# Kernel optimization log

Hardware: AMD Instinct MI355X
Metric: run time of the kernel (lower is better)

## Reference

```python
import jax, jax.numpy as jnp
import numpy as np

D_MODEL = 1024
D_HEAD = 64
B, S = 4, 2048


def setup_inputs() -> dict:
    key = jax.random.key(0)
    ks = jax.random.split(key, 4)
    scale = 1.0 / np.sqrt(D_MODEL)
    return {
        "embeddings": jax.random.normal(ks[0], (B, S, D_MODEL), dtype=jnp.float32),
        "Wq": jax.random.normal(ks[1], (D_MODEL, D_HEAD), dtype=jnp.float32) * scale,
        "bq": jnp.zeros((D_HEAD,), dtype=jnp.float32),
        "Wk": jax.random.normal(ks[2], (D_MODEL, D_HEAD), dtype=jnp.float32) * scale,
        "bk": jnp.zeros((D_HEAD,), dtype=jnp.float32),
        "Wv": jax.random.normal(ks[3], (D_MODEL, D_HEAD), dtype=jnp.float32) * scale,
        "bv": jnp.zeros((D_HEAD,), dtype=jnp.float32),
    }


def reference(embeddings, Wq, bq, Wk, bk, Wv, bv):
    # Q, K, V projections: (b, s, d_head)
    Q = embeddings @ Wq + bq
    K = embeddings @ Wk + bk
    V = embeddings @ Wv + bv
    # scaled scores: (b, s, s)
    scores = jnp.einsum("bqd,bkd->bqk", Q, K) / jnp.sqrt(jnp.float32(D_HEAD))
    # causal mask: positions k > q get -inf
    s = scores.shape[-1]
    causal = jnp.tril(jnp.ones((s, s), dtype=bool))
    scores = jnp.where(causal, scores, -jnp.inf)
    pattern = jax.nn.softmax(scores, axis=-1)
    # attention output: (b, s, d_head)  (note: original forward skips self.output)
    return jnp.einsum("bqk,bkd->bqd", pattern, V)
```

## Files before the change

### kernel.cpp

```cpp
#include <hip/hip_runtime.h>
#include <hip/hip_bf16.h>

#define DMODEL 1024
#define DH 64
#define BB 4
#define SS 2048
#define NROW (BB * SS)
#define NS 8

typedef __attribute__((ext_vector_type(8))) short bf16x8;
typedef __attribute__((ext_vector_type(4))) float f32x4;

__device__ __forceinline__ unsigned short f2bf(float f) {
    __hip_bfloat16 h = __float2bfloat16(f);
    return __builtin_bit_cast(unsigned short, h);
}

__global__ __launch_bounds__(256) void prep_wt_kernel(
    const float* __restrict__ Wq, const float* __restrict__ Wk,
    const float* __restrict__ Wv, unsigned short* __restrict__ Wt)
{
    __shared__ float T[64][65];
    const int tid = threadIdx.x;
    const int m   = blockIdx.x;
    const int k0  = blockIdx.y * 64;
    const float* W = (m == 0) ? Wq : (m == 1) ? Wk : Wv;

    const int tn = tid & 63, tk = tid >> 6;
    #pragma unroll
    for (int j = 0; j < 16; ++j)
        T[4 * j + tk][tn] = W[(size_t)(k0 + 4 * j + tk) * DH + tn];
    __syncthreads();

    const int wk = tid & 63, wn = tid >> 6;
    #pragma unroll
    for (int j = 0; j < 16; ++j)
        Wt[(size_t)(m * 64 + 4 * j + wn) * DMODEL + k0 + wk] =
            f2bf(T[wk][4 * j + wn]);
}

__global__ __launch_bounds__(256) void qkv_proj_mfma(
    const float* __restrict__ emb, const unsigned short* __restrict__ Wt,
    const float* __restrict__ bq, const float* __restrict__ bk,
    const float* __restrict__ bv,
    unsigned short* __restrict__ Q, unsigned short* __restrict__ K,
    unsigned short* __restrict__ V)
{
    __shared__ unsigned short Bs[4][3][48 * 64];

    const int tid  = threadIdx.x;
    const int lane = tid & 63;
    const int w    = tid >> 6;
    const int wr   = w >> 1;
    const int wc   = w & 1;
    const int c    = lane & 15;
    const int g    = lane >> 4;
    const int row0    = blockIdx.x * 32 + 16 * wr;
    const int colbase = blockIdx.y * 96 + 48 * wc;

    const int bj_row = lane >> 3;
    const int bj_sl  = (lane & 7) ^ (bj_row & 7);
    const unsigned short* wt_lane =
        Wt + (size_t)(colbase + bj_row) * DMODEL + 8 * bj_sl;

    const float* arow = emb + (size_t)(row0 + c) * DMODEL + 8 * g;

    f32x4 acc[3];
    #pragma unroll
    for (int t = 0; t < 3; ++t) acc[t] = (f32x4){0.f, 0.f, 0.f, 0.f};

    float4 a0[3], a1[3], a2[3], a3[3];

#define ISSUE(S, R) do {                                                     \
    _Pragma("unroll")                                                        \
    for (int j = 0; j < 6; ++j)                                              \
        __builtin_amdgcn_global_load_lds(                                    \
            (const __attribute__((address_space(1))) void*)(                 \
                wt_lane + (size_t)8 * (j) * DMODEL + 64 * (S)),              \
            (__attribute__((address_space(3))) void*)&Bs[w][R][(j) * 512],   \
            16, 0, 0);                                                       \
    a0[R] = *reinterpret_cast<const float4*>(arow + 64 * (S));               \
    a1[R] = *reinterpret_cast<const float4*>(arow + 64 * (S) + 4);           \
    a2[R] = *reinterpret_cast<const float4*>(arow + 64 * (S) + 32);          \
    a3[R] = *reinterpret_cast<const float4*>(arow + 64 * (S) + 36);          \
} while (0)

    ISSUE(0, 0);
    ISSUE(1, 1);

    #pragma unroll
    for (int s = 0; s < 16; ++s) {
        const int r = s % 3;
        if (s < 15) asm volatile("s_waitcnt vmcnt(10)" ::: "memory");
        else        asm volatile("s_waitcnt vmcnt(0)"  ::: "memory");
        __builtin_amdgcn_sched_barrier(0);

        if (s + 2 < 16) ISSUE(s + 2, (s + 2) % 3);

        bf16x8 af[2];
        {
            union { bf16x8 v; unsigned short u[8]; } p0, p1;
            p0.u[0] = f2bf(a0[r].x); p0.u[1] = f2bf(a0[r].y);
            p0.u[2] = f2bf(a0[r].z); p0.u[3] = f2bf(a0[r].w);
            p0.u[4] = f2bf(a1[r].x); p0.u[5] = f2bf(a1[r].y);
            p0.u[6] = f2bf(a1[r].z); p0.u[7] = f2bf(a1[r].w);
            p1.u[0] = f2bf(a2[r].x); p1.u[1] = f2bf(a2[r].y);
            p1.u[2] = f2bf(a2[r].z); p1.u[3] = f2bf(a2[r].w);
            p1.u[4] = f2bf(a3[r].x); p1.u[5] = f2bf(a3[r].y);
            p1.u[6] = f2bf(a3[r].z); p1.u[7] = f2bf(a3[r].w);
            af[0] = p0.v; af[1] = p1.v;
        }

        #pragma unroll
        for (int t = 0; t < 3; ++t)
            #pragma unroll
            for (int kp = 0; kp < 2; ++kp) {
                const int lrow = 16 * t + c;
                const int slot = (4 * kp + g) ^ (lrow & 7);
                bf16x8 bfr = __builtin_bit_cast(bf16x8,
                    *reinterpret_cast<const uint4*>(&Bs[w][r][lrow * 64 + slot * 8]));
                acc[t] = __builtin_amdgcn_mfma_f32_16x16x32_bf16(af[kp], bfr, acc[t], 0, 0, 0);
            }
    }
#undef ISSUE

    #pragma unroll
    for (int t = 0; t < 3; ++t) {
        const int col = colbase + 16 * t + c;
        const int m   = col >> 6;
        const int lc  = col & 63;
        const float* bias = (m == 0) ? bq : (m == 1) ? bk : bv;
        unsigned short* O = (m == 0) ? Q : (m == 1) ? K : V;
        const float bs    = bias[lc];
        const float scale = (m == 0) ? 0.125f : 1.0f;
        #pragma unroll
        for (int i = 0; i < 4; ++i) {
            const int rr = row0 + 4 * g + i;
            O[(size_t)rr * DH + lc] = f2bf((acc[t][i] + bs) * scale);
        }
    }
}

__global__ __launch_bounds__(256) void attn_mfma_split(
    const unsigned short* __restrict__ Q, const unsigned short* __restrict__ K,
    const unsigned short* __restrict__ V,
    float* __restrict__ Opart, float* __restrict__ mpart,
    float* __restrict__ lpart)
{
    __shared__ unsigned short Ks[64][72];
    __shared__ unsigned short Vt[64][72];
    __shared__ unsigned short Ps[4][16][72];

    const int tid  = threadIdx.x;
    const int lane = tid & 63;
    const int w    = tid >> 6;
    const int c    = lane & 15;
    const int g    = lane >> 4;
    const int qt   = blockIdx.x;
    const int b    = blockIdx.y;
    const int sp   = blockIdx.z;
    const int q0   = qt * 64;

    const int ntile = qt + 1;
    const int kt0 = (ntile * sp) / NS;
    const int kt1 = (ntile * (sp + 1)) / NS;

    const unsigned short* Qb = Q + (size_t)b * SS * DH;
    const unsigned short* Kb = K + (size_t)b * SS * DH;
    const unsigned short* Vb = V + (size_t)b * SS * DH;

    bf16x8 qa[2];
    #pragma unroll
    for (int kp = 0; kp < 2; ++kp)
        qa[kp] = __builtin_bit_cast(bf16x8,
            *reinterpret_cast<const uint4*>(
                &Qb[(size_t)(q0 + 16 * w + c) * DH + 32 * kp + 8 * g]));

    f32x4 o[4];
    #pragma unroll
    for (int t = 0; t < 4; ++t) o[t] = (f32x4){0.f, 0.f, 0.f, 0.f};
    float m_i = -1e30f;
    float l_i = 0.f;

    for (int kt = kt0; kt < kt1; ++kt) {
        const int kb0 = kt * 64;
        __syncthreads();
        #pragma unroll
        for (int j = 0; j < 2; ++j) {
            const int idx = tid + 256 * j;
            const int kv  = idx >> 3;
            const int m8  = idx & 7;
            const int d0  = m8 * 8;
            *reinterpret_cast<uint4*>(&Ks[kv][d0]) =
                *reinterpret_cast<const uint4*>(&Kb[(size_t)(kb0 + kv) * DH + d0]);
            const uint4 vv =
                *reinterpret_cast<const uint4*>(&Vb[(size_t)(kb0 + kv) * DH + d0]);
            const unsigned wd[4] = {vv.x, vv.y, vv.z, vv.w};
            #pragma unroll
            for (int e = 0; e < 8; ++e)
                Vt[(d0 + e) ^ m8][kv] =
                    (unsigned short)(wd[e >> 1] >> (16 * (e & 1)));
        }
        __syncthreads();

        f32x4 s[4];
        #pragma unroll
        for (int t = 0; t < 4; ++t) s[t] = (f32x4){0.f, 0.f, 0.f, 0.f};
        #pragma unroll
        for (int t = 0; t < 4; ++t)
            #pragma unroll
            for (int kp = 0; kp < 2; ++kp) {
                bf16x8 kf = __builtin_bit_cast(bf16x8,
                    *reinterpret_cast<const uint4*>(&Ks[16 * t + c][32 * kp + 8 * g]));
                s[t] = __builtin_amdgcn_mfma_f32_16x16x32_bf16(kf, qa[kp], s[t], 0, 0, 0);
            }

        if (kt == qt) {
            #pragma unroll
            for (int t = 0; t < 4; ++t)
                #pragma unroll
                for (int i = 0; i < 4; ++i)
                    if (16 * t + 4 * g + i > 16 * w + c) s[t][i] = -1e30f;
        }

        float mx = m_i;
        #pragma unroll
        for (int t = 0; t < 4; ++t)
            mx = fmaxf(mx, fmaxf(fmaxf(s[t][0], s[t][1]), fmaxf(s[t][2], s[t][3])));
        mx = fmaxf(mx, __shfl_xor(mx, 16));
        mx = fmaxf(mx, __shfl_xor(mx, 32));
        const float al = __expf(m_i - mx);
        m_i = mx;
        float sum = 0.f;
        #pragma unroll
        for (int t = 0; t < 4; ++t)
            #pragma unroll
            for (int i = 0; i < 4; ++i) {
                const float p = __expf(s[t][i] - mx);
                s[t][i] = p;
                sum += p;
            }
        sum += __shfl_xor(sum, 16);
        sum += __shfl_xor(sum, 32);
        l_i = l_i * al + sum;

        #pragma unroll
        for (int t = 0; t < 4; ++t) {
            uint2 u;
            u.x = (unsigned)f2bf(s[t][0]) | ((unsigned)f2bf(s[t][1]) << 16);
            u.y = (unsigned)f2bf(s[t][2]) | ((unsigned)f2bf(s[t][3]) << 16);
            *reinterpret_cast<uint2*>(&Ps[w][c][16 * t + 4 * g]) = u;
        }

        #pragma unroll
        for (int t = 0; t < 4; ++t)
            #pragma unroll
            for (int i = 0; i < 4; ++i)
                o[t][i] *= al;

        #pragma unroll
        for (int kp = 0; kp < 2; ++kp) {
            bf16x8 pb = __builtin_bit_cast(bf16x8,
                *reinterpret_cast<const uint4*>(&Ps[w][c][32 * kp + 8 * g]));
            #pragma unroll
            for (int t = 0; t < 4; ++t) {
                const int dv = 16 * t + c;
                const int pr = dv ^ ((2 * t + (c >> 3)) & 7);
                bf16x8 vf = __builtin_bit_cast(bf16x8,
                    *reinterpret_cast<const uint4*>(&Vt[pr][32 * kp + 8 * g]));
                o[t] = __builtin_amdgcn_mfma_f32_16x16x32_bf16(vf, pb, o[t], 0, 0, 0);
            }
        }
    }

    const int qrow = b * SS + q0 + 16 * w + c;
    #pragma unroll
    for (int t = 0; t < 4; ++t) {
        float4 v = {o[t][0], o[t][1], o[t][2], o[t][3]};
        *reinterpret_cast<float4*>(
            &Opart[((size_t)sp * NROW + qrow) * DH + 16 * t + 4 * g]) = v;
    }
    if (g == 0) {
        mpart[(size_t)sp * NROW + qrow] = m_i;
        lpart[(size_t)sp * NROW + qrow] = l_i;
    }
}

__global__ __launch_bounds__(256) void attn_combine(
    const float* __restrict__ Opart, const float* __restrict__ mpart,
    const float* __restrict__ lpart, float* __restrict__ out)
{
    const int idx = blockIdx.x * 256 + threadIdx.x;
    const int row = idx >> 4;
    const int d4  = (idx & 15) * 4;

    float m[NS];
    float M = -1e30f;
    #pragma unroll
    for (int s = 0; s < NS; ++s) {
        m[s] = mpart[(size_t)s * NROW + row];
        M = fmaxf(M, m[s]);
    }
    float L = 0.f;
    float4 acc = {0.f, 0.f, 0.f, 0.f};
    #pragma unroll
    for (int s = 0; s < NS; ++s) {
        const float wgt = __expf(m[s] - M);
        L += wgt * lpart[(size_t)s * NROW + row];
        const float4 p = *reinterpret_cast<const float4*>(
            &Opart[((size_t)s * NROW + row) * DH + d4]);
        acc.x += wgt * p.x; acc.y += wgt * p.y;
        acc.z += wgt * p.z; acc.w += wgt * p.w;
    }
    const float inv = 1.f / L;
    float4 r = {acc.x * inv, acc.y * inv, acc.z * inv, acc.w * inv};
    *reinterpret_cast<float4*>(&out[(size_t)row * DH + d4]) = r;
}

extern "C" void kernel_launch(void* const* d_in, const int* in_sizes, int n_in,
                              void* d_out, int out_size, void* d_ws, size_t ws_size,
                              hipStream_t stream) {
    const float* emb = (const float*)d_in[0];
    const float* Wq  = (const float*)d_in[1];
    const float* bq  = (const float*)d_in[2];
    const float* Wk  = (const float*)d_in[3];
    const float* bk  = (const float*)d_in[4];
    const float* Wv  = (const float*)d_in[5];
    const float* bv  = (const float*)d_in[6];
    float* out = (float*)d_out;

    unsigned short* Qw = (unsigned short*)d_ws;
    unsigned short* Kw = Qw + (size_t)NROW * DH;
    unsigned short* Vw = Kw + (size_t)NROW * DH;
    unsigned short* Wt = Vw + (size_t)NROW * DH;
    float* Opart = (float*)(Wt + (size_t)192 * DMODEL);
    float* mpart = Opart + (size_t)NS * NROW * DH;
    float* lpart = mpart + (size_t)NS * NROW;

    hipLaunchKernelGGL(prep_wt_kernel, dim3(3, 16), dim3(256), 0, stream,
                       Wq, Wk, Wv, Wt);
    hipLaunchKernelGGL(qkv_proj_mfma, dim3(NROW / 32, 2), dim3(256), 0, stream,
                       emb, Wt, bq, bk, bv, Qw, Kw, Vw);
    hipLaunchKernelGGL(attn_mfma_split, dim3(SS / 64, BB, NS), dim3(256), 0, stream,
                       Qw, Kw, Vw, Opart, mpart, lpart);
    hipLaunchKernelGGL(attn_combine, dim3(NROW * 16 / 256), dim3(256), 0, stream,
                       Opart, mpart, lpart, out);
}
```

Baseline: 53.42 us.

## Double-buffer V tiles, read K directly from global, store partial outputs as bf16

The split attention kernel now keeps a double-buffered transposed V tile in shared memory and prefetches the next V tile into registers while the current tile is computed. This leaves one barrier per iteration instead of two. K fragments are loaded straight from global memory into MFMA operands rather than staged through LDS. Partial outputs are written as bf16 instead of fp32, halving the traffic between the split and combine kernels, at the cost of some precision and more uncoalesced global K loads.

Result: slower. 56.50 us (+5.8%).

```diff
diff --git a/kernel.cpp b/kernel.cpp
--- a/kernel.cpp
+++ b/kernel.cpp
@@ -14,6 +14,10 @@
 __device__ __forceinline__ unsigned short f2bf(float f) {
     __hip_bfloat16 h = __float2bfloat16(f);
     return __builtin_bit_cast(unsigned short, h);
+}
+__device__ __forceinline__ float bf2f(unsigned short u) {
+    unsigned v = (unsigned)u << 16;
+    return __builtin_bit_cast(float, v);
 }
 
 __global__ __launch_bounds__(256) void prep_wt_kernel(
@@ -144,11 +148,10 @@
 __global__ __launch_bounds__(256) void attn_mfma_split(
     const unsigned short* __restrict__ Q, const unsigned short* __restrict__ K,
     const unsigned short* __restrict__ V,
-    float* __restrict__ Opart, float* __restrict__ mpart,
+    unsigned short* __restrict__ Opart, float* __restrict__ mpart,
     float* __restrict__ lpart)
 {
-    __shared__ unsigned short Ks[64][72];
-    __shared__ unsigned short Vt[64][72];
+    __shared__ unsigned short Vt[2][64][72];
     __shared__ unsigned short Ps[4][16][72];
 
     const int tid  = threadIdx.x;
@@ -182,112 +185,137 @@
     float m_i = -1e30f;
     float l_i = 0.f;
 
-    for (int kt = kt0; kt < kt1; ++kt) {
-        const int kb0 = kt * 64;
+    const int kv0 = tid >> 3;
+    const int m8  = tid & 7;
+    const int d0  = m8 * 8;
+    uint4 vreg[2];
+
+#define VLOAD(KT) do {                                                        \
+    vreg[0] = *reinterpret_cast<const uint4*>(                                \
+        &Vb[(size_t)((KT) * 64 + kv0) * DH + d0]);                            \
+    vreg[1] = *reinterpret_cast<const uint4*>(                                \
+        &Vb[(size_t)((KT) * 64 + kv0 + 32) * DH + d0]);                       \
+} while (0)
+
+#define VWRITE(BI) do {                                                       \
+    _Pragma("unroll")                                                         \
+    for (int j = 0; j < 2; ++j) {                                             \
+        const int kv = kv0 + 32 * j;                                          \
+        const unsigned wd[4] = {vreg[j].x, vreg[j].y, vreg[j].z, vreg[j].w};  \
+        _Pragma("unroll")                                                     \
+        for (int e = 0; e < 8; ++e)                                           \
+            Vt[BI][(d0 + e) ^ m8][kv] =                                       \
+                (unsigned short)(wd[e >> 1] >> (16 * (e & 1)));               \
+    }                                                                         \
+} while (0)
+
+    if (kt0 < kt1) {
+        VLOAD(kt0);
+        VWRITE(0);
         __syncthreads();
-        #pragma unroll
-        for (int j = 0; j < 2; ++j) {
-            const int idx = tid + 256 * j;
-            const int kv  = idx >> 3;
-            const int m8  = idx & 7;
-            const int d0  = m8 * 8;
-            *reinterpret_cast<uint4*>(&Ks[kv][d0]) =
-                *reinterpret_cast<const uint4*>(&Kb[(size_t)(kb0 + kv) * DH + d0]);
-            const uint4 vv =
-                *reinterpret_cast<const uint4*>(&Vb[(size_t)(kb0 + kv) * DH + d0]);
-            const unsigned wd[4] = {vv.x, vv.y, vv.z, vv.w};
-            #pragma unroll
-            for (int e = 0; e < 8; ++e)
-                Vt[(d0 + e) ^ m8][kv] =
-                    (unsigned short)(wd[e >> 1] >> (16 * (e & 1)));
+
+        for (int kt = kt0; kt < kt1; ++kt) {
+            const int kb0 = kt * 64;
+            const int cur = (kt - kt0) & 1;
+            const bool havenext = (kt + 1 < kt1);
+            if (havenext) VLOAD(kt + 1);
+
+            f32x4 s[4];
+            #pragma unroll
+            for (int t = 0; t < 4; ++t) s[t] = (f32x4){0.f, 0.f, 0.f, 0.f};
+            #pragma unroll
+            for (int t = 0; t < 4; ++t)
+                #pragma unroll
+                for (int kp = 0; kp < 2; ++kp) {
+                    bf16x8 kf = __builtin_bit_cast(bf16x8,
+                        *reinterpret_cast<const uint4*>(
+                            &Kb[(size_t)(kb0 + 16 * t + c) * DH + 32 * kp + 8 * g]));
+                    s[t] = __builtin_amdgcn_mfma_f32_16x16x32_bf16(kf, qa[kp], s[t], 0, 0, 0);
+                }
+
+            if (kt == qt) {
+                #pragma unroll
+                for (int t = 0; t < 4; ++t)
+                    #pragma unroll
+                    for (int i = 0; i < 4; ++i)
+                        if (16 * t + 4 * g + i > 16 * w + c) s[t][i] = -1e30f;
+            }
+
+            float mx = m_i;
+            #pragma unroll
+            for (int t = 0; t < 4; ++t)
+                mx = fmaxf(mx, fmaxf(fmaxf(s[t][0], s[t][1]), fmaxf(s[t][2], s[t][3])));
+            mx = fmaxf(mx, __shfl_xor(mx, 16));
+            mx = fmaxf(mx, __shfl_xor(mx, 32));
+            const float al = __expf(m_i - mx);
+            m_i = mx;
+            float sum = 0.f;
+            #pragma unroll
+            for (int t = 0; t < 4; ++t)
+                #pragma unroll
+                for (int i = 0; i < 4; ++i) {
+                    const float p = __expf(s[t][i] - mx);
+                    s[t][i] = p;
+                    sum += p;
+                }
+            sum += __shfl_xor(sum, 16);
+            sum += __shfl_xor(sum, 32);
+            l_i = l_i * al + sum;
+
+            #pragma unroll
+            for (int t = 0; t < 4; ++t) {
+                uint2 u;
+                u.x = (unsigned)f2bf(s[t][0]) | ((unsigned)f2bf(s[t][1]) << 16);
+                u.y = (unsigned)f2bf(s[t][2]) | ((unsigned)f2bf(s[t][3]) << 16);
+                *reinterpret_cast<uint2*>(&Ps[w][c][16 * t + 4 * g]) = u;
+            }
+
+            #pragma unroll
+            for (int t = 0; t < 4; ++t)
+                #pragma unroll
+                for (int i = 0; i < 4; ++i)
+                    o[t][i] *= al;
+
+            #pragma unroll
+            for (int kp = 0; kp < 2; ++kp) {
+                bf16x8 pb = __builtin_bit_cast(bf16x8,
+                    *reinterpret_cast<const uint4*>(&Ps[w][c][32 * kp + 8 * g]));
+                #pragma unroll
+                for (int t = 0; t < 4; ++t) {
+                    const int dv = 16 * t + c;
+                    const int pr = dv ^ ((2 * t + (c >> 3)) & 7);
+                    bf16x8 vf = __builtin_bit_cast(bf16x8,
+                        *reinterpret_cast<const uint4*>(&Vt[cur][pr][32 * kp + 8 * g]));
+                    o[t] = __builtin_amdgcn_mfma_f32_16x16x32_bf16(vf, pb, o[t], 0, 0, 0);
+                }
+            }
+
+            if (havenext) {
+                VWRITE(cur ^ 1);
+                __syncthreads();
+            }
         }
-        __syncthreads();
-
-        f32x4 s[4];
-        #pragma unroll
-        for (int t = 0; t < 4; ++t) s[t] = (f32x4){0.f, 0.f, 0.f, 0.f};
-        #pragma unroll
-        for (int t = 0; t < 4; ++t)
-            #pragma unroll
-            for (int kp = 0; kp < 2; ++kp) {
-                bf16x8 kf = __builtin_bit_cast(bf16x8,
-                    *reinterpret_cast<const uint4*>(&Ks[16 * t + c][32 * kp + 8 * g]));
-                s[t] = __builtin_amdgcn_mfma_f32_16x16x32_bf16(kf, qa[kp], s[t], 0, 0, 0);
-            }
-
-        if (kt == qt) {
-            #pragma unroll
-            for (int t = 0; t < 4; ++t)
-                #pragma unroll
-                for (int i = 0; i < 4; ++i)
-                    if (16 * t + 4 * g + i > 16 * w + c) s[t][i] = -1e30f;
-        }
-
-        float mx = m_i;
-        #pragma unroll
-        for (int t = 0; t < 4; ++t)
-            mx = fmaxf(mx, fmaxf(fmaxf(s[t][0], s[t][1]), fmaxf(s[t][2], s[t][3])));
-        mx = fmaxf(mx, __shfl_xor(mx, 16));
-        mx = fmaxf(mx, __shfl_xor(mx, 32));
-        const float al = __expf(m_i - mx);
-        m_i = mx;
-        float sum = 0.f;
-        #pragma unroll
-        for (int t = 0; t < 4; ++t)
-            #pragma unroll
-            for (int i = 0; i < 4; ++i) {
-                const float p = __expf(s[t][i] - mx);
-                s[t][i] = p;
-                sum += p;
-            }
-        sum += __shfl_xor(sum, 16);
-        sum += __shfl_xor(sum, 32);
-        l_i = l_i * al + sum;
-
-        #pragma unroll
-        for (int t = 0; t < 4; ++t) {
-            uint2 u;
-            u.x = (unsigned)f2bf(s[t][0]) | ((unsigned)f2bf(s[t][1]) << 16);
-            u.y = (unsigned)f2bf(s[t][2]) | ((unsigned)f2bf(s[t][3]) << 16);
-            *reinterpret_cast<uint2*>(&Ps[w][c][16 * t + 4 * g]) = u;
-        }
-
-        #pragma unroll
-        for (int t = 0; t < 4; ++t)
-            #pragma unroll
-            for (int i = 0; i < 4; ++i)
-                o[t][i] *= al;
-
-        #pragma unroll
-        for (int kp = 0; kp < 2; ++kp) {
-            bf16x8 pb = __builtin_bit_cast(bf16x8,
-                *reinterpret_cast<const uint4*>(&Ps[w][c][32 * kp + 8 * g]));
-            #pragma unroll
-            for (int t = 0; t < 4; ++t) {
-                const int dv = 16 * t + c;
-                const int pr = dv ^ ((2 * t + (c >> 3)) & 7);
-                bf16x8 vf = __builtin_bit_cast(bf16x8,
-                    *reinterpret_cast<const uint4*>(&Vt[pr][32 * kp + 8 * g]));
-                o[t] = __builtin_amdgcn_mfma_f32_16x16x32_bf16(vf, pb, o[t], 0, 0, 0);
-            }
-        }
     }
 
     const int qrow = b * SS + q0 + 16 * w + c;
     #pragma unroll
     for (int t = 0; t < 4; ++t) {
-        float4 v = {o[t][0], o[t][1], o[t][2], o[t][3]};
-        *reinterpret_cast<float4*>(
-            &Opart[((size_t)sp * NROW + qrow) * DH + 16 * t + 4 * g]) = v;
+        uint2 u;
+        u.x = (unsigned)f2bf(o[t][0]) | ((unsigned)f2bf(o[t][1]) << 16);
+        u.y = (unsigned)f2bf(o[t][2]) | ((unsigned)f2bf(o[t][3]) << 16);
+        *reinterpret_cast<uint2*>(
+            &Opart[((size_t)sp * NROW + qrow) * DH + 16 * t + 4 * g]) = u;
     }
     if (g == 0) {
         mpart[(size_t)sp * NROW + qrow] = m_i;
         lpart[(size_t)sp * NROW + qrow] = l_i;
     }
+#undef VLOAD
+#undef VWRITE
 }
 
 __global__ __launch_bounds__(256) void attn_combine(
-    const float* __restrict__ Opart, const float* __restrict__ mpart,
+    const unsigned short* __restrict__ Opart, const float* __restrict__ mpart,
     const float* __restrict__ lpart, float* __restrict__ out)
 {
     const int idx = blockIdx.x * 256 + threadIdx.x;
@@ -307,10 +335,12 @@
     for (int s = 0; s < NS; ++s) {
         const float wgt = __expf(m[s] - M);
         L += wgt * lpart[(size_t)s * NROW + row];
-        const float4 p = *reinterpret_cast<const float4*>(
+        const uint2 pu = *reinterpret_cast<const uint2*>(
             &Opart[((size_t)s * NROW + row) * DH + d4]);
-        acc.x += wgt * p.x; acc.y += wgt * p.y;
-        acc.z += wgt * p.z; acc.w += wgt * p.w;
+        acc.x += wgt * bf2f((unsigned short)(pu.x & 0xffff));
+        acc.y += wgt * bf2f((unsigned short)(pu.x >> 16));
+        acc.z += wgt * bf2f((unsigned short)(pu.y & 0xffff));
+        acc.w += wgt * bf2f((unsigned short)(pu.y >> 16));
     }
     const float inv = 1.f / L;
     float4 r = {acc.x * inv, acc.y * inv, acc.z * inv, acc.w * inv};
@@ -333,8 +363,8 @@
     unsigned short* Kw = Qw + (size_t)NROW * DH;
     unsigned short* Vw = Kw + (size_t)NROW * DH;
     unsigned short* Wt = Vw + (size_t)NROW * DH;
-    float* Opart = (float*)(Wt + (size_t)192 * DMODEL);
-    float* mpart = Opart + (size_t)NS * NROW * DH;
+    unsigned short* Opart = Wt + (size_t)192 * DMODEL;
+    float* mpart = (float*)(Opart + (size_t)NS * NROW * DH);
     float* lpart = mpart + (size_t)NS * NROW;
 
     hipLaunchKernelGGL(prep_wt_kernel, dim3(3, 16), dim3(256), 0, stream,
```

## Split QKV projection over K into two halves with separate reduce-finish kernel

Applied to the files above, without the earlier changes.

The QKV projection now splits the 1024-long reduction into two halves along a new grid z dimension, which doubles the number of blocks. Each half writes fp32 partial sums to a workspace. A new qkv_finish kernel adds the halves, applies bias and the Q scale, and converts to bf16. The LDS staging via global_load_lds is dropped: B fragments are loaded straight into registers with double buffering, and the explicit waitcnt pipeline is removed. This trades extra fp32 partial-sum traffic and one more kernel launch for more parallelism and simpler loads.

After: 73.74 us. 38.0% more time.

```diff
diff --git a/kernel.cpp b/kernel.cpp
--- a/kernel.cpp
+++ b/kernel.cpp
@@ -41,13 +41,8 @@
 
 __global__ __launch_bounds__(256) void qkv_proj_mfma(
     const float* __restrict__ emb, const unsigned short* __restrict__ Wt,
-    const float* __restrict__ bq, const float* __restrict__ bk,
-    const float* __restrict__ bv,
-    unsigned short* __restrict__ Q, unsigned short* __restrict__ K,
-    unsigned short* __restrict__ V)
-{
-    __shared__ unsigned short Bs[4][3][48 * 64];
-
+    float* __restrict__ Cpart)
+{
     const int tid  = threadIdx.x;
     const int lane = tid & 63;
     const int w    = tid >> 6;
@@ -55,90 +50,98 @@
     const int wc   = w & 1;
     const int c    = lane & 15;
     const int g    = lane >> 4;
-    const int row0    = blockIdx.x * 32 + 16 * wr;
-    const int colbase = blockIdx.y * 96 + 48 * wc;
-
-    const int bj_row = lane >> 3;
-    const int bj_sl  = (lane & 7) ^ (bj_row & 7);
-    const unsigned short* wt_lane =
-        Wt + (size_t)(colbase + bj_row) * DMODEL + 8 * bj_sl;
-
-    const float* arow = emb + (size_t)(row0 + c) * DMODEL + 8 * g;
+    const int row0 = blockIdx.x * 32 + 16 * wr;
+    const int col0 = blockIdx.y * 96 + 48 * wc;
+    const int h    = blockIdx.z;
+    const int kbase = h * 512;
+
+    const float* arow = emb + (size_t)(row0 + c) * DMODEL + kbase + 8 * g;
+    const unsigned short* brow = Wt + (size_t)(col0 + c) * DMODEL + kbase + 8 * g;
 
     f32x4 acc[3];
     #pragma unroll
     for (int t = 0; t < 3; ++t) acc[t] = (f32x4){0.f, 0.f, 0.f, 0.f};
 
-    float4 a0[3], a1[3], a2[3], a3[3];
-
-#define ISSUE(S, R) do {                                                     \
+    float4 aA0, aA1, aA2, aA3, aB0, aB1, aB2, aB3;
+    uint4 bA[3][2], bB[3][2];
+
+#define LOADA(S, x0, x1, x2, x3) do {                                        \
+    x0 = *reinterpret_cast<const float4*>(arow + 64 * (S));                  \
+    x1 = *reinterpret_cast<const float4*>(arow + 64 * (S) + 4);              \
+    x2 = *reinterpret_cast<const float4*>(arow + 64 * (S) + 32);             \
+    x3 = *reinterpret_cast<const float4*>(arow + 64 * (S) + 36);             \
+} while (0)
+#define LOADB(S, bb) do {                                                    \
     _Pragma("unroll")                                                        \
-    for (int j = 0; j < 6; ++j)                                              \
-        __builtin_amdgcn_global_load_lds(                                    \
-            (const __attribute__((address_space(1))) void*)(                 \
-                wt_lane + (size_t)8 * (j) * DMODEL + 64 * (S)),              \
-            (__attribute__((address_space(3))) void*)&Bs[w][R][(j) * 512],   \
-            16, 0, 0);                                                       \
-    a0[R] = *reinterpret_cast<const float4*>(arow + 64 * (S));               \
-    a1[R] = *reinterpret_cast<const float4*>(arow + 64 * (S) + 4);           \
-    a2[R] = *reinterpret_cast<const float4*>(arow + 64 * (S) + 32);          \
-    a3[R] = *reinterpret_cast<const float4*>(arow + 64 * (S) + 36);          \
+    for (int t = 0; t < 3; ++t)                                              \
+        _Pragma("unroll")                                                    \
+        for (int kp = 0; kp < 2; ++kp)                                       \
+            bb[t][kp] = *reinterpret_cast<const uint4*>(                     \
+                brow + (size_t)(16 * t) * DMODEL + 64 * (S) + 32 * kp);      \
 } while (0)
-
-    ISSUE(0, 0);
-    ISSUE(1, 1);
-
-    #pragma unroll
-    for (int s = 0; s < 16; ++s) {
-        const int r = s % 3;
-        if (s < 15) asm volatile("s_waitcnt vmcnt(10)" ::: "memory");
-        else        asm volatile("s_waitcnt vmcnt(0)"  ::: "memory");
-        __builtin_amdgcn_sched_barrier(0);
-
-        if (s + 2 < 16) ISSUE(s + 2, (s + 2) % 3);
-
-        bf16x8 af[2];
-        {
-            union { bf16x8 v; unsigned short u[8]; } p0, p1;
-            p0.u[0] = f2bf(a0[r].x); p0.u[1] = f2bf(a0[r].y);
-            p0.u[2] = f2bf(a0[r].z); p0.u[3] = f2bf(a0[r].w);
-            p0.u[4] = f2bf(a1[r].x); p0.u[5] = f2bf(a1[r].y);
-            p0.u[6] = f2bf(a1[r].z); p0.u[7] = f2bf(a1[r].w);
-            p1.u[0] = f2bf(a2[r].x); p1.u[1] = f2bf(a2[r].y);
-            p1.u[2] = f2bf(a2[r].z); p1.u[3] = f2bf(a2[r].w);
-            p1.u[4] = f2bf(a3[r].x); p1.u[5] = f2bf(a3[r].y);
-            p1.u[6] = f2bf(a3[r].z); p1.u[7] = f2bf(a3[r].w);
-            af[0] = p0.v; af[1] = p1.v;
-        }
-
-        #pragma unroll
-        for (int t = 0; t < 3; ++t)
-            #pragma unroll
-            for (int kp = 0; kp < 2; ++kp) {
-                const int lrow = 16 * t + c;
-                const int slot = (4 * kp + g) ^ (lrow & 7);
-                bf16x8 bfr = __builtin_bit_cast(bf16x8,
-                    *reinterpret_cast<const uint4*>(&Bs[w][r][lrow * 64 + slot * 8]));
-                acc[t] = __builtin_amdgcn_mfma_f32_16x16x32_bf16(af[kp], bfr, acc[t], 0, 0, 0);
-            }
-    }
-#undef ISSUE
-
-    #pragma unroll
-    for (int t = 0; t < 3; ++t) {
-        const int col = colbase + 16 * t + c;
-        const int m   = col >> 6;
-        const int lc  = col & 63;
-        const float* bias = (m == 0) ? bq : (m == 1) ? bk : bv;
-        unsigned short* O = (m == 0) ? Q : (m == 1) ? K : V;
-        const float bs    = bias[lc];
-        const float scale = (m == 0) ? 0.125f : 1.0f;
-        #pragma unroll
-        for (int i = 0; i < 4; ++i) {
-            const int rr = row0 + 4 * g + i;
-            O[(size_t)rr * DH + lc] = f2bf((acc[t][i] + bs) * scale);
-        }
-    }
+#define CONSUME(x0, x1, x2, x3, bb) do {                                     \
+    bf16x8 af[2];                                                            \
+    union { bf16x8 v; unsigned short u[8]; } p0, p1;                         \
+    p0.u[0] = f2bf(x0.x); p0.u[1] = f2bf(x0.y);                              \
+    p0.u[2] = f2bf(x0.z); p0.u[3] = f2bf(x0.w);                              \
+    p0.u[4] = f2bf(x1.x); p0.u[5] = f2bf(x1.y);                              \
+    p0.u[6] = f2bf(x1.z); p0.u[7] = f2bf(x1.w);                              \
+    p1.u[0] = f2bf(x2.x); p1.u[1] = f2bf(x2.y);                              \
+    p1.u[2] = f2bf(x2.z); p1.u[3] = f2bf(x2.w);                              \
+    p1.u[4] = f2bf(x3.x); p1.u[5] = f2bf(x3.y);                              \
+    p1.u[6] = f2bf(x3.z); p1.u[7] = f2bf(x3.w);                              \
+    af[0] = p0.v; af[1] = p1.v;                                              \
+    _Pragma("unroll")                                                        \
+    for (int t = 0; t < 3; ++t) {                                            \
+        acc[t] = __builtin_amdgcn_mfma_f32_16x16x32_bf16(                    \
+            af[0], __builtin_bit_cast(bf16x8, bb[t][0]), acc[t], 0, 0, 0);   \
+        acc[t] = __builtin_amdgcn_mfma_f32_16x16x32_bf16(                    \
+            af[1], __builtin_bit_cast(bf16x8, bb[t][1]), acc[t], 0, 0, 0);   \
+    }                                                                        \
+} while (0)
+
+    LOADA(0, aA0, aA1, aA2, aA3);
+    LOADB(0, bA);
+
+    #pragma unroll
+    for (int s = 0; s < 8; ++s) {
+        if ((s & 1) == 0) {
+            if (s + 1 < 8) { LOADA(s + 1, aB0, aB1, aB2, aB3); LOADB(s + 1, bB); }
+            CONSUME(aA0, aA1, aA2, aA3, bA);
+        } else {
+            if (s + 1 < 8) { LOADA(s + 1, aA0, aA1, aA2, aA3); LOADB(s + 1, bA); }
+            CONSUME(aB0, aB1, aB2, aB3, bB);
+        }
+    }
+#undef LOADA
+#undef LOADB
+#undef CONSUME
+
+    float* Cp = Cpart + (size_t)h * NROW * 192;
+    #pragma unroll
+    for (int t = 0; t < 3; ++t)
+        #pragma unroll
+        for (int i = 0; i < 4; ++i)
+            Cp[(size_t)(row0 + 4 * g + i) * 192 + col0 + 16 * t + c] = acc[t][i];
+}
+
+__global__ __launch_bounds__(192) void qkv_finish(
+    const float* __restrict__ Cpart,
+    const float* __restrict__ bq, const float* __restrict__ bk,
+    const float* __restrict__ bv,
+    unsigned short* __restrict__ Q, unsigned short* __restrict__ K,
+    unsigned short* __restrict__ V)
+{
+    const int row = blockIdx.x;
+    const int col = threadIdx.x;
+    const float v = Cpart[(size_t)row * 192 + col]
+                  + Cpart[(size_t)NROW * 192 + (size_t)row * 192 + col];
+    const int m  = col >> 6;
+    const int lc = col & 63;
+    const float* bias = (m == 0) ? bq : (m == 1) ? bk : bv;
+    unsigned short* O = (m == 0) ? Q : (m == 1) ? K : V;
+    const float scale = (m == 0) ? 0.125f : 1.0f;
+    O[(size_t)row * DH + lc] = f2bf((v + bias[lc]) * scale);
 }
 
 __global__ __launch_bounds__(256) void attn_mfma_split(
@@ -333,14 +336,17 @@
     unsigned short* Kw = Qw + (size_t)NROW * DH;
     unsigned short* Vw = Kw + (size_t)NROW * DH;
     unsigned short* Wt = Vw + (size_t)NROW * DH;
-    float* Opart = (float*)(Wt + (size_t)192 * DMODEL);
+    float* Cpart = (float*)(Wt + (size_t)192 * DMODEL);
+    float* Opart = Cpart + (size_t)2 * NROW * 192;
     float* mpart = Opart + (size_t)NS * NROW * DH;
     float* lpart = mpart + (size_t)NS * NROW;
 
     hipLaunchKernelGGL(prep_wt_kernel, dim3(3, 16), dim3(256), 0, stream,
                        Wq, Wk, Wv, Wt);
-    hipLaunchKernelGGL(qkv_proj_mfma, dim3(NROW / 32, 2), dim3(256), 0, stream,
-                       emb, Wt, bq, bk, bv, Qw, Kw, Vw);
+    hipLaunchKernelGGL(qkv_proj_mfma, dim3(NROW / 32, 2, 2), dim3(256), 0, stream,
+                       emb, Wt, Cpart);
+    hipLaunchKernelGGL(qkv_finish, dim3(NROW), dim3(192), 0, stream,
+                       Cpart, bq, bk, bv, Qw, Kw, Vw);
     hipLaunchKernelGGL(attn_mfma_split, dim3(SS / 64, BB, NS), dim3(256), 0, stream,
                        Qw, Kw, Vw, Opart, mpart, lpart);
     hipLaunchKernelGGL(attn_combine, dim3(NROW * 16 / 256), dim3(256), 0, stream,
```

## Share weight tile across warps in QKV projection with 64-row blocks

Applied to the files above, without the earlier changes.

The QKV projection kernel now stages a 96x512 bf16 weight chunk in LDS shared by all four warps, instead of each warp streaming its own 48-column slice. Each warp computes 16 rows by 96 columns (six accumulators), and the grid is halved to 64 rows per block. This cuts redundant weight traffic and LDS fills per output, and A loads use a 4-deep register pipeline. In exchange, the weight load is no longer overlapped with compute: each of the two K-chunks waits on vmcnt(0) plus a barrier. LDS use grows to 96KB per block, which lowers occupancy.

Result: faster. 49.47 us (-7.4%).

```diff
diff --git a/kernel.cpp b/kernel.cpp
--- a/kernel.cpp
+++ b/kernel.cpp
@@ -46,86 +46,88 @@
     unsigned short* __restrict__ Q, unsigned short* __restrict__ K,
     unsigned short* __restrict__ V)
 {
-    __shared__ unsigned short Bs[4][3][48 * 64];
+    __shared__ unsigned short Bs[96 * 512];
 
     const int tid  = threadIdx.x;
     const int lane = tid & 63;
     const int w    = tid >> 6;
-    const int wr   = w >> 1;
-    const int wc   = w & 1;
     const int c    = lane & 15;
     const int g    = lane >> 4;
-    const int row0    = blockIdx.x * 32 + 16 * wr;
-    const int colbase = blockIdx.y * 96 + 48 * wc;
-
-    const int bj_row = lane >> 3;
-    const int bj_sl  = (lane & 7) ^ (bj_row & 7);
-    const unsigned short* wt_lane =
-        Wt + (size_t)(colbase + bj_row) * DMODEL + 8 * bj_sl;
-
-    const float* arow = emb + (size_t)(row0 + c) * DMODEL + 8 * g;
-
-    f32x4 acc[3];
-    #pragma unroll
-    for (int t = 0; t < 3; ++t) acc[t] = (f32x4){0.f, 0.f, 0.f, 0.f};
-
-    float4 a0[3], a1[3], a2[3], a3[3];
-
-#define ISSUE(S, R) do {                                                     \
-    _Pragma("unroll")                                                        \
-    for (int j = 0; j < 6; ++j)                                              \
-        __builtin_amdgcn_global_load_lds(                                    \
-            (const __attribute__((address_space(1))) void*)(                 \
-                wt_lane + (size_t)8 * (j) * DMODEL + 64 * (S)),              \
-            (__attribute__((address_space(3))) void*)&Bs[w][R][(j) * 512],   \
-            16, 0, 0);                                                       \
-    a0[R] = *reinterpret_cast<const float4*>(arow + 64 * (S));               \
-    a1[R] = *reinterpret_cast<const float4*>(arow + 64 * (S) + 4);           \
-    a2[R] = *reinterpret_cast<const float4*>(arow + 64 * (S) + 32);          \
-    a3[R] = *reinterpret_cast<const float4*>(arow + 64 * (S) + 36);          \
+    const int row0    = blockIdx.x * 64;
+    const int colbase = blockIdx.y * 96;
+
+    const float* arow = emb + (size_t)(row0 + 16 * w + c) * DMODEL + 8 * g;
+
+    f32x4 acc[6];
+    #pragma unroll
+    for (int t = 0; t < 6; ++t) acc[t] = (f32x4){0.f, 0.f, 0.f, 0.f};
+
+    float4 aR[4][4];
+
+#define LOADA(KC, S, R) do {                                                  \
+    aR[R][0] = *reinterpret_cast<const float4*>(arow + (KC)*512 + 64*(S));    \
+    aR[R][1] = *reinterpret_cast<const float4*>(arow + (KC)*512 + 64*(S) + 4);\
+    aR[R][2] = *reinterpret_cast<const float4*>(arow + (KC)*512 + 64*(S) + 32);\
+    aR[R][3] = *reinterpret_cast<const float4*>(arow + (KC)*512 + 64*(S) + 36);\
 } while (0)
 
-    ISSUE(0, 0);
-    ISSUE(1, 1);
-
-    #pragma unroll
-    for (int s = 0; s < 16; ++s) {
-        const int r = s % 3;
-        if (s < 15) asm volatile("s_waitcnt vmcnt(10)" ::: "memory");
-        else        asm volatile("s_waitcnt vmcnt(0)"  ::: "memory");
+    #pragma unroll
+    for (int kc = 0; kc < 2; ++kc) {
+        #pragma unroll
+        for (int j = 0; j < 24; ++j) {
+            const int r = 4 * j + w;
+            __builtin_amdgcn_global_load_lds(
+                (const __attribute__((address_space(1))) void*)(
+                    Wt + (size_t)(colbase + r) * DMODEL + kc * 512
+                       + 8 * (lane ^ (r & 7))),
+                (__attribute__((address_space(3))) void*)&Bs[r * 512],
+                16, 0, 0);
+        }
+        asm volatile("s_waitcnt vmcnt(0)" ::: "memory");
         __builtin_amdgcn_sched_barrier(0);
-
-        if (s + 2 < 16) ISSUE(s + 2, (s + 2) % 3);
-
-        bf16x8 af[2];
-        {
-            union { bf16x8 v; unsigned short u[8]; } p0, p1;
-            p0.u[0] = f2bf(a0[r].x); p0.u[1] = f2bf(a0[r].y);
-            p0.u[2] = f2bf(a0[r].z); p0.u[3] = f2bf(a0[r].w);
-            p0.u[4] = f2bf(a1[r].x); p0.u[5] = f2bf(a1[r].y);
-            p0.u[6] = f2bf(a1[r].z); p0.u[7] = f2bf(a1[r].w);
-            p1.u[0] = f2bf(a2[r].x); p1.u[1] = f2bf(a2[r].y);
-            p1.u[2] = f2bf(a2[r].z); p1.u[3] = f2bf(a2[r].w);
-            p1.u[4] = f2bf(a3[r].x); p1.u[5] = f2bf(a3[r].y);
-            p1.u[6] = f2bf(a3[r].z); p1.u[7] = f2bf(a3[r].w);
-            af[0] = p0.v; af[1] = p1.v;
-        }
-
-        #pragma unroll
-        for (int t = 0; t < 3; ++t)
-            #pragma unroll
-            for (int kp = 0; kp < 2; ++kp) {
-                const int lrow = 16 * t + c;
-                const int slot = (4 * kp + g) ^ (lrow & 7);
-                bf16x8 bfr = __builtin_bit_cast(bf16x8,
-                    *reinterpret_cast<const uint4*>(&Bs[w][r][lrow * 64 + slot * 8]));
-                acc[t] = __builtin_amdgcn_mfma_f32_16x16x32_bf16(af[kp], bfr, acc[t], 0, 0, 0);
+        __syncthreads();
+
+        LOADA(kc, 0, 0);
+        LOADA(kc, 1, 1);
+        LOADA(kc, 2, 2);
+
+        #pragma unroll
+        for (int s = 0; s < 8; ++s) {
+            const int r = s & 3;
+            if (s + 3 < 8) LOADA(kc, s + 3, (s + 3) & 3);
+
+            bf16x8 af[2];
+            {
+                union { bf16x8 v; unsigned short u[8]; } p0, p1;
+                p0.u[0] = f2bf(aR[r][0].x); p0.u[1] = f2bf(aR[r][0].y);
+                p0.u[2] = f2bf(aR[r][0].z); p0.u[3] = f2bf(aR[r][0].w);
+                p0.u[4] = f2bf(aR[r][1].x); p0.u[5] = f2bf(aR[r][1].y);
+                p0.u[6] = f2bf(aR[r][1].z); p0.u[7] = f2bf(aR[r][1].w);
+                p1.u[0] = f2bf(aR[r][2].x); p1.u[1] = f2bf(aR[r][2].y);
+                p1.u[2] = f2bf(aR[r][2].z); p1.u[3] = f2bf(aR[r][2].w);
+                p1.u[4] = f2bf(aR[r][3].x); p1.u[5] = f2bf(aR[r][3].y);
+                p1.u[6] = f2bf(aR[r][3].z); p1.u[7] = f2bf(aR[r][3].w);
+                af[0] = p0.v; af[1] = p1.v;
             }
-    }
-#undef ISSUE
-
-    #pragma unroll
-    for (int t = 0; t < 3; ++t) {
+
+            #pragma unroll
+            for (int t = 0; t < 6; ++t)
+                #pragma unroll
+                for (int kp = 0; kp < 2; ++kp) {
+                    const int row  = 16 * t + c;
+                    const int slot = (8 * s + 4 * kp + g) ^ (row & 7);
+                    bf16x8 bfr = __builtin_bit_cast(bf16x8,
+                        *reinterpret_cast<const uint4*>(&Bs[row * 512 + slot * 8]));
+                    acc[t] = __builtin_amdgcn_mfma_f32_16x16x32_bf16(
+                        af[kp], bfr, acc[t], 0, 0, 0);
+                }
+        }
+        if (kc == 0) __syncthreads();
+    }
+#undef LOADA
+
+    #pragma unroll
+    for (int t = 0; t < 6; ++t) {
         const int col = colbase + 16 * t + c;
         const int m   = col >> 6;
         const int lc  = col & 63;
@@ -135,7 +137,7 @@
         const float scale = (m == 0) ? 0.125f : 1.0f;
         #pragma unroll
         for (int i = 0; i < 4; ++i) {
-            const int rr = row0 + 4 * g + i;
+            const int rr = row0 + 16 * w + 4 * g + i;
             O[(size_t)rr * DH + lc] = f2bf((acc[t][i] + bs) * scale);
         }
     }
@@ -339,7 +341,7 @@
 
     hipLaunchKernelGGL(prep_wt_kernel, dim3(3, 16), dim3(256), 0, stream,
                        Wq, Wk, Wv, Wt);
-    hipLaunchKernelGGL(qkv_proj_mfma, dim3(NROW / 32, 2), dim3(256), 0, stream,
+    hipLaunchKernelGGL(qkv_proj_mfma, dim3(NROW / 64, 2), dim3(256), 0, stream,
                        emb, Wt, bq, bk, bv, Qw, Kw, Vw);
     hipLaunchKernelGGL(attn_mfma_split, dim3(SS / 64, BB, NS), dim3(256), 0, stream,
                        Qw, Kw, Vw, Opart, mpart, lpart);
```
